# Optimization experiments

Hardware: AMD Instinct MI355X
Metric: run time of the kernel (lower is better)

Reference implementation:

```python
import jax, jax.numpy as jnp
import numpy as np

N_EMBD = 2048
N_HEAD = 16
HEAD_DIM = N_EMBD // N_HEAD
B, T = 4, 2048
EPS = 1e-5


def layer_norm(x, w, b):
    mu = jnp.mean(x, axis=-1, keepdims=True)
    var = jnp.var(x, axis=-1, keepdims=True)
    return (x - mu) * jax.lax.rsqrt(var + EPS) * w + b


def setup_inputs() -> dict:
    key = jax.random.key(0)
    ks = jax.random.split(key, 8)
    s = 0.02
    return {
        "x": jax.random.normal(ks[0], (B, T, N_EMBD), dtype=jnp.float32),
        "ln1_w": jnp.ones((N_EMBD,), jnp.float32),
        "ln1_b": jnp.zeros((N_EMBD,), jnp.float32),
        "attn_w": jax.random.normal(ks[1], (N_EMBD, 3 * N_EMBD), jnp.float32) * s,
        "attn_b": jnp.zeros((3 * N_EMBD,), jnp.float32),
        "ln2_w": jnp.ones((N_EMBD,), jnp.float32),
        "ln2_b": jnp.zeros((N_EMBD,), jnp.float32),
        "fc_w": jax.random.normal(ks[2], (N_EMBD, 4 * N_EMBD), jnp.float32) * s,
        "fc_b": jnp.zeros((4 * N_EMBD,), jnp.float32),
        "proj_w": jax.random.normal(ks[3], (4 * N_EMBD, N_EMBD), jnp.float32) * s,
        "proj_b": jnp.zeros((N_EMBD,), jnp.float32),
    }


def reference(x, ln1_w, ln1_b, attn_w, attn_b, ln2_w, ln2_b, fc_w, fc_b, proj_w, proj_b):
    b, t, c = x.shape
    # --- causal self-attention on ln_1(x); note: source Block has NO residual
    # and attention's c_proj is never invoked in the original forward. ---
    h = layer_norm(x, ln1_w, ln1_b)
    qkv = h @ attn_w + attn_b                      # [B,T,3C]
    q, k, v = jnp.split(qkv, 3, axis=-1)
    q = q.reshape(b, t, N_HEAD, HEAD_DIM)
    k = k.reshape(b, t, N_HEAD, HEAD_DIM)
    v = v.reshape(b, t, N_HEAD, HEAD_DIM)
    scale = 1.0 / np.sqrt(HEAD_DIM).astype(np.float32)
    scores = jnp.einsum("bqhd,bkhd->bhqk", q, k) * scale   # [B,H,T,T]
    causal = jnp.tril(jnp.ones((t, t), dtype=bool))
    scores = jnp.where(causal, scores, -jnp.inf)
    attn = jax.nn.softmax(scores, axis=-1)
    y = jnp.einsum("bhqk,bkhd->bqhd", attn, v).reshape(b, t, c)
    # --- MLP on ln_2(y); again no residual in the source Block ---
    h2 = layer_norm(y, ln2_w, ln2_b)
    out = jax.nn.gelu(h2 @ fc_w + fc_b, approximate=False) @ proj_w + proj_b
    return out
```

## Files before the change

kernel.cpp:

```cpp
#include <hip/hip_runtime.h>
#include <hip/hip_bf16.h>

typedef __attribute__((ext_vector_type(8))) short      bf16x8;
typedef __attribute__((ext_vector_type(4))) float      f32x4;
typedef __attribute__((ext_vector_type(8))) unsigned short u16x8;

__device__ __forceinline__ unsigned short f2bf(float f) {
    union { __hip_bfloat16 h; unsigned short u; } cv;
    cv.h = __float2bfloat16(f);
    return cv.u;
}
__device__ __forceinline__ float bf2f(unsigned short u) {
    union { float f; unsigned int i; } cv;
    cv.i = ((unsigned int)u) << 16;
    return cv.f;
}
__device__ __forceinline__ void gload_lds16(const void* g, void* l) {
    __builtin_amdgcn_global_load_lds(
        (const __attribute__((address_space(1))) void*)g,
        (__attribute__((address_space(3))) void*)l, 16, 0, 0);
}
__device__ __forceinline__ f32x4 mfma16(bf16x8 a, bf16x8 b, f32x4 c) {
    return __builtin_amdgcn_mfma_f32_16x16x32_bf16(a, b, c, 0, 0, 0);
}
__device__ __forceinline__ float gelu_f(float x) {
    return 0.5f * x * (1.0f + erff(x * 0.70710678118654752f));
}

#define S_BARRIER() asm volatile("s_barrier" ::: "memory")
#define LGKM0()     do { asm volatile("s_waitcnt lgkmcnt(0)" ::: "memory"); \
                         __builtin_amdgcn_sched_barrier(0); } while (0)

template<int IN_BF16>
__global__ __launch_bounds__(256) void ln_kernel(const void* in, const float* w, const float* b,
                                                 unsigned short* out) {
    const int row = blockIdx.x;
    const int tid = threadIdx.x;
    float v[8];
    if constexpr (IN_BF16) {
        const unsigned short* p = (const unsigned short*)in + (size_t)row * 2048 + tid * 8;
        u16x8 raw = *(const u16x8*)p;
#pragma unroll
        for (int j = 0; j < 8; j++) v[j] = bf2f(raw[j]);
    } else {
        const float* p = (const float*)in + (size_t)row * 2048 + tid * 8;
        float4 a = ((const float4*)p)[0];
        float4 c = ((const float4*)p)[1];
        v[0] = a.x; v[1] = a.y; v[2] = a.z; v[3] = a.w;
        v[4] = c.x; v[5] = c.y; v[6] = c.z; v[7] = c.w;
    }
    float s = 0.f, ss = 0.f;
#pragma unroll
    for (int j = 0; j < 8; j++) { s += v[j]; ss += v[j] * v[j]; }
#pragma unroll
    for (int off = 32; off > 0; off >>= 1) {
        s  += __shfl_xor(s, off);
        ss += __shfl_xor(ss, off);
    }
    __shared__ float red[8];
    const int wid = tid >> 6, lane = tid & 63;
    if (lane == 0) { red[wid] = s; red[4 + wid] = ss; }
    __syncthreads();
    s  = red[0] + red[1] + red[2] + red[3];
    ss = red[4] + red[5] + red[6] + red[7];
    const float mean = s * (1.0f / 2048.0f);
    const float var  = ss * (1.0f / 2048.0f) - mean * mean;
    const float rstd = rsqrtf(var + 1e-5f);
    unsigned short* op = out + (size_t)row * 2048 + tid * 8;
    u16x8 ov;
#pragma unroll
    for (int j = 0; j < 8; j++) {
        int c = tid * 8 + j;
        ov[j] = f2bf((v[j] - mean) * rstd * w[c] + b[c]);
    }
    *(u16x8*)op = ov;
}

__global__ __launch_bounds__(256) void wt_kernel(const float* W, unsigned short* WT, int K, int N) {
    __shared__ unsigned short sm[32][33];
    const int n0 = blockIdx.x * 32, k0 = blockIdx.y * 32;
    const int tx = threadIdx.x, ty = threadIdx.y;
#pragma unroll
    for (int i = 0; i < 4; i++) {
        int k = ty + i * 8;
        sm[k][tx] = f2bf(W[(size_t)(k0 + k) * N + n0 + tx]);
    }
    __syncthreads();
#pragma unroll
    for (int i = 0; i < 4; i++) {
        int n = ty + i * 8;
        WT[(size_t)(n0 + n) * K + k0 + tx] = sm[tx][n];
    }
}

__global__ __launch_bounds__(256) void vt_kernel(const unsigned short* qkv, unsigned short* vT) {
    __shared__ unsigned short sm[32][33];
    const int t0 = blockIdx.x * 32, d0 = blockIdx.y * 32, bh = blockIdx.z;
    const int b = bh >> 4, h = bh & 15;
    const int tx = threadIdx.x, ty = threadIdx.y;
#pragma unroll
    for (int i = 0; i < 4; i++) {
        int t = ty + i * 8;
        sm[t][tx] = qkv[(size_t)(b * 2048 + t0 + t) * 6144 + 4096 + h * 128 + d0 + tx];
    }
    __syncthreads();
#pragma unroll
    for (int i = 0; i < 4; i++) {
        int d = ty + i * 8;
        vT[(size_t)(bh * 128 + d0 + d) * 2048 + t0 + tx] = sm[tx][d];
    }
}

template<int OUT_BF16, int ACT_GELU>
__global__ __launch_bounds__(512, 2) void gemm256(const unsigned short* __restrict__ A,
                                                  const unsigned short* __restrict__ BT,
                                                  const float* __restrict__ bias,
                                                  void* __restrict__ Cout,
                                                  int M, int N, int K) {
    __shared__ unsigned short As[2][256 * 64];
    __shared__ unsigned short Bs[2][256 * 64];
    const int tid = threadIdx.x;
    const int gx = gridDim.x;
    const int lin = blockIdx.y * gx + blockIdx.x;
    const int cpx = (gx * gridDim.y) >> 3;
    const int swz = (lin & 7) * cpx + (lin >> 3);
    const int n0 = (swz % gx) * 256, m0 = (swz / gx) * 256;

    const int wid = tid >> 6, lane = tid & 63;
    const int wr = wid >> 2, wc = wid & 3;
    const int lg = lane >> 4, l15 = lane & 15;
    const int nkt = K >> 6;

    const int sr = tid >> 3;
    const int scol = ((tid & 7) ^ (sr & 7)) * 8;
    const int sdst = tid * 8;

    auto stageA = [&](int ta, int h) {
        const unsigned short* g = A + (size_t)(m0 + h * 128 + sr) * K + ta * 64 + scol;
        unsigned short* d = &As[ta & 1][h * 8192 + sdst];
        gload_lds16(g, d);
        gload_lds16(g + (size_t)64 * K, d + 4096);
    };
    auto stageB = [&](int ta, int h) {
        const unsigned short* g = BT + (size_t)(n0 + h * 128 + sr) * K + ta * 64 + scol;
        unsigned short* d = &Bs[ta & 1][h * 8192 + sdst];
        gload_lds16(g, d);
        gload_lds16(g + (size_t)64 * K, d + 4096);
    };

    stageA(0, 0); stageA(0, 1); stageB(0, 0); stageB(0, 1);
    if (nkt > 1) {
        stageB(1, 0); stageB(1, 1); stageA(1, 0);
        asm volatile("s_waitcnt vmcnt(6)" ::: "memory");
    } else {
        asm volatile("s_waitcnt vmcnt(0)" ::: "memory");
    }
    S_BARRIER();

    f32x4 acc[8][4] = {};
    const int lxor = l15 & 7;
    const int co0 = (lg ^ lxor) * 8;
    const int co1 = ((4 + lg) ^ lxor) * 8;
    const int arow0 = wr * 64 + l15;
    const int brow = wc * 64 + l15;

#define GPHASE(MH, CO, BQ, READB, STAGE_STMT, TAIL_STMT)                          \
    do {                                                                          \
        bf16x8 af[4];                                                             \
        _Pragma("unroll")                                                         \
        for (int i = 0; i < 4; i++)                                               \
            af[i] = *(const bf16x8*)&Ap[((MH) * 128 + arow0 + i * 16) * 64 + (CO)];\
        if (READB) {                                                              \
            _Pragma("unroll")                                                     \
            for (int n = 0; n < 4; n++)                                           \
                BQ[n] = *(const bf16x8*)&Bp[(brow + n * 16) * 64 + (CO)];         \
        }                                                                         \
        STAGE_STMT;                                                               \
        S_BARRIER();                                                              \
        LGKM0();                                                                  \
        __builtin_amdgcn_s_setprio(1);                                            \
        _Pragma("unroll")                                                         \
        for (int i = 0; i < 4; i++) {                                             \
            _Pragma("unroll")                                                     \
            for (int n = 0; n < 4; n++)                                           \
                acc[(MH) * 4 + i][n] = mfma16(af[i], BQ[n], acc[(MH) * 4 + i][n]);\
        }                                                                         \
        __builtin_amdgcn_s_setprio(0);                                            \
        TAIL_STMT;                                                                \
        S_BARRIER();                                                              \
    } while (0)

    for (int t = 0; t < nkt; ++t) {
        const int p = t & 1;
        const unsigned short* Ap = As[p];
        const unsigned short* Bp = Bs[p];
        bf16x8 bq0[4], bq1[4];
        const bool steady = (t < nkt - 2);

        GPHASE(0, co0, bq0, 1,
               if (t + 1 < nkt) stageA(t + 1, 1),
               (void)0);
        GPHASE(0, co1, bq1, 1, (void)0,
               if (steady) asm volatile("s_waitcnt vmcnt(8)" ::: "memory");
               else        asm volatile("s_waitcnt vmcnt(0)" ::: "memory"));
        GPHASE(1, co0, bq0, 0,
               if (t + 2 < nkt) { stageB(t + 2, 0); stageB(t + 2, 1); stageA(t + 2, 0); },
               (void)0);
        GPHASE(1, co1, bq1, 0, (void)0,
               if (steady) asm volatile("s_waitcnt vmcnt(8)" ::: "memory");
               else        asm volatile("s_waitcnt vmcnt(0)" ::: "memory"));
    }
#undef GPHASE

#pragma unroll
    for (int n = 0; n < 4; n++) {
        const int col = n0 + wc * 64 + n * 16 + l15;
        const float bv = bias[col];
#pragma unroll
        for (int m = 0; m < 8; m++) {
            const int rbase = m0 + (m >> 2) * 128 + wr * 64 + (m & 3) * 16 + lg * 4;
#pragma unroll
            for (int r = 0; r < 4; r++) {
                float v = acc[m][n][r] + bv;
                if (ACT_GELU) v = gelu_f(v);
                if (OUT_BF16)
                    ((unsigned short*)Cout)[(size_t)(rbase + r) * N + col] = f2bf(v);
                else
                    ((float*)Cout)[(size_t)(rbase + r) * N + col] = v;
            }
        }
    }
}

__global__ __launch_bounds__(256) void attn_kernel(const unsigned short* __restrict__ qkv,
                                                   const unsigned short* __restrict__ vT,
                                                   unsigned short* __restrict__ y) {
    __shared__ unsigned short Qs[64 * 128];
    __shared__ unsigned short Ks[64 * 128];
    __shared__ unsigned short VTs[128 * 64];
    const int pair = blockIdx.x, h = blockIdx.y, b = blockIdx.z;
    const int tid = threadIdx.x, wid = tid >> 6, lane = tid & 63;
    const int lg = lane >> 4, l15 = lane & 15;
    const float scale = 0.08838834764831845f;
    unsigned short* Ps = &Qs[wid * 1024];

    for (int pass = 0; pass < 2; pass++) {
        const int qt = (pass == 0) ? (31 - pair) : pair;
        __syncthreads();
#pragma unroll
        for (int i = 0; i < 4; i++) {
            int idx = tid + 256 * i;
            int row = idx >> 4, ch = idx & 15;
            const unsigned short* g = qkv + (size_t)(b * 2048 + qt * 64 + row) * 6144
                                      + h * 128 + ((ch ^ (row & 7)) * 8);
            gload_lds16(g, &Qs[idx * 8]);
        }
        __syncthreads();
        const int rq = wid * 16 + l15;
        bf16x8 qf[4];
#pragma unroll
        for (int c = 0; c < 4; c++)
            qf[c] = *(const bf16x8*)&Qs[rq * 128 + (((c * 4 + lg) ^ (rq & 7)) * 8)];

        float m_run[4], l_run[4];
#pragma unroll
        for (int r = 0; r < 4; r++) { m_run[r] = -1e30f; l_run[r] = 0.f; }
        f32x4 O[8] = {};

        const int nkb = qt + 1;
        for (int kb = 0; kb < nkb; kb++) {
            __syncthreads();
#pragma unroll
            for (int i = 0; i < 4; i++) {
                int idx = tid + 256 * i;
                int row = idx >> 4, ch = idx & 15;
                const unsigned short* g = qkv + (size_t)(b * 2048 + kb * 64 + row) * 6144
                                          + 2048 + h * 128 + ((ch ^ (row & 7)) * 8);
                gload_lds16(g, &Ks[idx * 8]);
            }
#pragma unroll
            for (int i = 0; i < 4; i++) {
                int idx = tid + 256 * i;
                int row = idx >> 3, ch = idx & 7;
                const unsigned short* g = vT + (size_t)((b * 16 + h) * 128 + row) * 2048
                                          + kb * 64 + ((ch ^ (row & 7)) * 8);
                gload_lds16(g, &VTs[idx * 8]);
            }
            __syncthreads();

            f32x4 S[4] = {};
#pragma unroll
            for (int n = 0; n < 4; n++) {
                const int rk = n * 16 + l15;
#pragma unroll
                for (int c = 0; c < 4; c++) {
                    bf16x8 kf = *(const bf16x8*)&Ks[rk * 128 + (((c * 4 + lg) ^ (rk & 7)) * 8)];
                    S[n] = mfma16(qf[c], kf, S[n]);
                }
            }

            const int qgb = qt * 64 + wid * 16 + lg * 4;
#pragma unroll
            for (int r = 0; r < 4; r++) {
                const int qg = qgb + r;
                float sv[4];
#pragma unroll
                for (int n = 0; n < 4; n++) {
                    const int kg = kb * 64 + n * 16 + l15;
                    sv[n] = (kg <= qg) ? S[n][r] * scale : -1e30f;
                }
                float mx = fmaxf(fmaxf(sv[0], sv[1]), fmaxf(sv[2], sv[3]));
                mx = fmaxf(mx, __shfl_xor(mx, 1));
                mx = fmaxf(mx, __shfl_xor(mx, 2));
                mx = fmaxf(mx, __shfl_xor(mx, 4));
                mx = fmaxf(mx, __shfl_xor(mx, 8));
                const float mnew = fmaxf(m_run[r], mx);
                const float f = __expf(m_run[r] - mnew);
                const float p0 = __expf(sv[0] - mnew), p1 = __expf(sv[1] - mnew);
                const float p2 = __expf(sv[2] - mnew), p3 = __expf(sv[3] - mnew);
                float rs = (p0 + p1) + (p2 + p3);
                rs += __shfl_xor(rs, 1);
                rs += __shfl_xor(rs, 2);
                rs += __shfl_xor(rs, 4);
                rs += __shfl_xor(rs, 8);
                l_run[r] = l_run[r] * f + rs;
                m_run[r] = mnew;
#pragma unroll
                for (int n2 = 0; n2 < 8; n2++) O[n2][r] *= f;
                const int prow = lg * 4 + r;
                const int pxor = (prow & 7) << 3;
                Ps[(prow * 64 + l15) ^ pxor]      = f2bf(p0);
                Ps[(prow * 64 + 16 + l15) ^ pxor] = f2bf(p1);
                Ps[(prow * 64 + 32 + l15) ^ pxor] = f2bf(p2);
                Ps[(prow * 64 + 48 + l15) ^ pxor] = f2bf(p3);
            }

#pragma unroll
            for (int kk = 0; kk < 2; kk++) {
                bf16x8 pf = *(const bf16x8*)&Ps[l15 * 64 + (((kk * 4 + lg) ^ (l15 & 7)) * 8)];
#pragma unroll
                for (int n2 = 0; n2 < 8; n2++) {
                    const int rv = n2 * 16 + l15;
                    bf16x8 vf = *(const bf16x8*)&VTs[rv * 64 + (((kk * 4 + lg) ^ (rv & 7)) * 8)];
                    O[n2] = mfma16(pf, vf, O[n2]);
                }
            }
        }

#pragma unroll
        for (int r = 0; r < 4; r++) {
            const float inv = 1.0f / l_run[r];
            const size_t row = (size_t)(b * 2048 + qt * 64 + wid * 16 + lg * 4 + r);
#pragma unroll
            for (int n2 = 0; n2 < 8; n2++)
                y[row * 2048 + h * 128 + n2 * 16 + l15] = f2bf(O[n2][r] * inv);
        }
    }
}

extern "C" void kernel_launch(void* const* d_in, const int* in_sizes, int n_in,
                              void* d_out, int out_size, void* d_ws, size_t ws_size,
                              hipStream_t stream) {
    const float* x      = (const float*)d_in[0];
    const float* ln1_w  = (const float*)d_in[1];
    const float* ln1_b  = (const float*)d_in[2];
    const float* attn_w = (const float*)d_in[3];
    const float* attn_b = (const float*)d_in[4];
    const float* ln2_w  = (const float*)d_in[5];
    const float* ln2_b  = (const float*)d_in[6];
    const float* fc_w   = (const float*)d_in[7];
    const float* fc_b   = (const float*)d_in[8];
    const float* proj_w = (const float*)d_in[9];
    const float* proj_b = (const float*)d_in[10];
    float* out = (float*)d_out;

    char* ws = (char*)d_ws;
    const size_t MB = 1024ull * 1024ull;
    unsigned short* Wt   = (unsigned short*)(ws + 0);
    unsigned short* X1   = (unsigned short*)(ws + 32 * MB);
    unsigned short* X2   = (unsigned short*)(ws + 64 * MB);
    unsigned short* QKV  = (unsigned short*)(ws + 96 * MB);
    unsigned short* VT   = (unsigned short*)(ws + 192 * MB);
    unsigned short* Abuf = (unsigned short*)(ws + 96 * MB);

    ln_kernel<0><<<8192, 256, 0, stream>>>(x, ln1_w, ln1_b, X1);
    wt_kernel<<<dim3(6144 / 32, 2048 / 32), dim3(32, 8), 0, stream>>>(attn_w, Wt, 2048, 6144);
    gemm256<1, 0><<<dim3(24, 32), 512, 0, stream>>>(X1, Wt, attn_b, QKV, 8192, 6144, 2048);
    vt_kernel<<<dim3(64, 4, 64), dim3(32, 8), 0, stream>>>(QKV, VT);
    attn_kernel<<<dim3(16, 16, 4), 256, 0, stream>>>(QKV, VT, X2);
    ln_kernel<1><<<8192, 256, 0, stream>>>(X2, ln2_w, ln2_b, X1);
    wt_kernel<<<dim3(8192 / 32, 2048 / 32), dim3(32, 8), 0, stream>>>(fc_w, Wt, 2048, 8192);
    gemm256<1, 1><<<dim3(32, 32), 512, 0, stream>>>(X1, Wt, fc_b, Abuf, 8192, 8192, 2048);
    wt_kernel<<<dim3(2048 / 32, 8192 / 32), dim3(32, 8), 0, stream>>>(proj_w, Wt, 8192, 2048);
    gemm256<0, 0><<<dim3(8, 32), 512, 0, stream>>>(Abuf, Wt, proj_b, out, 8192, 2048, 8192);
}
```

Measured before the change: 1.072 ms.

## Restructure GEMM main loop into two half-phases with fewer barriers

Replaces the four-phase GPHASE macro, which had two barriers and a hard LDS wait plus sched_barrier per phase, with two half-iterations that each issue both K sub-slices of LDS reads and MFMAs. There are now two barriers per K-tile instead of eight, and the compiler is left free to interleave LDS reads with MFMAs. vmcnt waits are reorganised to match the new staging points. This cuts barrier and wait overhead but relies on the compiler's scheduling and makes the buffer-reuse hazards tighter.

```diff
diff --git a/kernel.cpp b/kernel.cpp
--- a/kernel.cpp
+++ b/kernel.cpp
@@ -27,9 +27,9 @@
     return 0.5f * x * (1.0f + erff(x * 0.70710678118654752f));
 }
 
-#define S_BARRIER() asm volatile("s_barrier" ::: "memory")
-#define LGKM0()     do { asm volatile("s_waitcnt lgkmcnt(0)" ::: "memory"); \
-                         __builtin_amdgcn_sched_barrier(0); } while (0)
+#define S_BARRIER()  asm volatile("s_barrier" ::: "memory")
+#define LGKM_SOFT()  asm volatile("s_waitcnt lgkmcnt(0)" ::: "memory")
+#define VMCNT(N)     asm volatile("s_waitcnt vmcnt(" #N ")" ::: "memory")
 
 template<int IN_BF16>
 __global__ __launch_bounds__(256) void ln_kernel(const void* in, const float* w, const float* b,
@@ -151,9 +151,9 @@
     stageA(0, 0); stageA(0, 1); stageB(0, 0); stageB(0, 1);
     if (nkt > 1) {
         stageB(1, 0); stageB(1, 1); stageA(1, 0);
-        asm volatile("s_waitcnt vmcnt(6)" ::: "memory");
+        VMCNT(6);
     } else {
-        asm volatile("s_waitcnt vmcnt(0)" ::: "memory");
+        VMCNT(0);
     }
     S_BARRIER();
 
@@ -164,53 +164,64 @@
     const int arow0 = wr * 64 + l15;
     const int brow = wc * 64 + l15;
 
-#define GPHASE(MH, CO, BQ, READB, STAGE_STMT, TAIL_STMT)                          \
-    do {                                                                          \
-        bf16x8 af[4];                                                             \
-        _Pragma("unroll")                                                         \
-        for (int i = 0; i < 4; i++)                                               \
-            af[i] = *(const bf16x8*)&Ap[((MH) * 128 + arow0 + i * 16) * 64 + (CO)];\
-        if (READB) {                                                              \
-            _Pragma("unroll")                                                     \
-            for (int n = 0; n < 4; n++)                                           \
-                BQ[n] = *(const bf16x8*)&Bp[(brow + n * 16) * 64 + (CO)];         \
-        }                                                                         \
-        STAGE_STMT;                                                               \
-        S_BARRIER();                                                              \
-        LGKM0();                                                                  \
-        __builtin_amdgcn_s_setprio(1);                                            \
-        _Pragma("unroll")                                                         \
-        for (int i = 0; i < 4; i++) {                                             \
-            _Pragma("unroll")                                                     \
-            for (int n = 0; n < 4; n++)                                           \
-                acc[(MH) * 4 + i][n] = mfma16(af[i], BQ[n], acc[(MH) * 4 + i][n]);\
-        }                                                                         \
-        __builtin_amdgcn_s_setprio(0);                                            \
-        TAIL_STMT;                                                                \
-        S_BARRIER();                                                              \
-    } while (0)
-
     for (int t = 0; t < nkt; ++t) {
         const int p = t & 1;
         const unsigned short* Ap = As[p];
         const unsigned short* Bp = Bs[p];
-        bf16x8 bq0[4], bq1[4];
-        const bool steady = (t < nkt - 2);
-
-        GPHASE(0, co0, bq0, 1,
-               if (t + 1 < nkt) stageA(t + 1, 1),
-               (void)0);
-        GPHASE(0, co1, bq1, 1, (void)0,
-               if (steady) asm volatile("s_waitcnt vmcnt(8)" ::: "memory");
-               else        asm volatile("s_waitcnt vmcnt(0)" ::: "memory"));
-        GPHASE(1, co0, bq0, 0,
-               if (t + 2 < nkt) { stageB(t + 2, 0); stageB(t + 2, 1); stageA(t + 2, 0); },
-               (void)0);
-        GPHASE(1, co1, bq1, 0, (void)0,
-               if (steady) asm volatile("s_waitcnt vmcnt(8)" ::: "memory");
-               else        asm volatile("s_waitcnt vmcnt(0)" ::: "memory"));
-    }
-#undef GPHASE
+        bf16x8 a0[4], a1[4], bq0[4], bq1[4];
+
+        if (t + 1 < nkt) stageA(t + 1, 1);
+#pragma unroll
+        for (int i = 0; i < 4; i++)
+            a0[i] = *(const bf16x8*)&Ap[(arow0 + i * 16) * 64 + co0];
+#pragma unroll
+        for (int n = 0; n < 4; n++)
+            bq0[n] = *(const bf16x8*)&Bp[(brow + n * 16) * 64 + co0];
+        __builtin_amdgcn_s_setprio(1);
+#pragma unroll
+        for (int i = 0; i < 4; i++)
+#pragma unroll
+            for (int n = 0; n < 4; n++)
+                acc[i][n] = mfma16(a0[i], bq0[n], acc[i][n]);
+#pragma unroll
+        for (int i = 0; i < 4; i++)
+            a1[i] = *(const bf16x8*)&Ap[(arow0 + i * 16) * 64 + co1];
+#pragma unroll
+        for (int n = 0; n < 4; n++)
+            bq1[n] = *(const bf16x8*)&Bp[(brow + n * 16) * 64 + co1];
+#pragma unroll
+        for (int i = 0; i < 4; i++)
+#pragma unroll
+            for (int n = 0; n < 4; n++)
+                acc[i][n] = mfma16(a1[i], bq1[n], acc[i][n]);
+        __builtin_amdgcn_s_setprio(0);
+        LGKM_SOFT();
+        S_BARRIER();
+
+        if (t + 2 < nkt) { stageB(t + 2, 0); stageB(t + 2, 1); stageA(t + 2, 0); }
+#pragma unroll
+        for (int i = 0; i < 4; i++)
+            a0[i] = *(const bf16x8*)&Ap[(128 + arow0 + i * 16) * 64 + co0];
+        __builtin_amdgcn_s_setprio(1);
+#pragma unroll
+        for (int i = 0; i < 4; i++)
+#pragma unroll
+            for (int n = 0; n < 4; n++)
+                acc[4 + i][n] = mfma16(a0[i], bq0[n], acc[4 + i][n]);
+#pragma unroll
+        for (int i = 0; i < 4; i++)
+            a1[i] = *(const bf16x8*)&Ap[(128 + arow0 + i * 16) * 64 + co1];
+#pragma unroll
+        for (int i = 0; i < 4; i++)
+#pragma unroll
+            for (int n = 0; n < 4; n++)
+                acc[4 + i][n] = mfma16(a1[i], bq1[n], acc[4 + i][n]);
+        __builtin_amdgcn_s_setprio(0);
+        LGKM_SOFT();
+        if (t + 2 < nkt)      VMCNT(6);
+        else if (t + 1 < nkt) VMCNT(0);
+        S_BARRIER();
+    }
 
 #pragma unroll
     for (int n = 0; n < 4; n++) {
```

After: 1.078 ms. No clear change (+0.6%).
